# Kernel optimization log

Measured on AMD Instinct MI355X. Metric: run time of the kernel, lower is better.

The kernel has to match this reference:

```python
import jax, jax.numpy as jnp
import numpy as np

NEG_INF = -1e9


def setup_inputs() -> dict:
    key = jax.random.key(0)
    ks = jax.random.split(key, 7)
    N, Q, C = 16, 4096, 77
    D, Dc, H, S = 512, 768, 8, 64
    scale = 0.02
    return {
        "query": jax.random.normal(ks[0], (N, Q, D), jnp.float32),
        "context": jax.random.normal(ks[1], (N, C, Dc), jnp.float32),
        "Wq": jax.random.normal(ks[2], (D, H, S), jnp.float32) * scale,
        "Wk": jax.random.normal(ks[3], (Dc, H, S), jnp.float32) * scale,
        "Wv": jax.random.normal(ks[4], (Dc, H, S), jnp.float32) * scale,
        "Wo": jax.random.normal(ks[5], (H, S, D), jnp.float32) * scale,
        "bo": jnp.zeros((D,), jnp.float32),
    }


def reference(query, context, Wq, Wk, Wv, Wo, bo):
    # Projections: split hidden dim into heads.
    q = jnp.einsum('NQD,DHS->NQHS', query, Wq)      # [N,Q,H,S]
    k = jnp.einsum('NCD,DHS->NCHS', context, Wk)    # [N,C,H,S]
    v = jnp.einsum('NCD,DHS->NCHS', context, Wv)    # [N,C,H,S]
    size_per_head = q.shape[-1]
    # Attention scores [N,H,Q,C], scaled by 1/sqrt(S).
    scores = jnp.einsum('NQHS,NCHS->NHQC', q, k) * (size_per_head ** -0.5)
    weights = jax.nn.softmax(scores, axis=3)
    out = jnp.einsum('NHQC,NCHS->NQHS', weights, v)  # [N,Q,H,S]
    # Merge heads back to model dim with output bias.
    return jnp.einsum('NQHS,HSD->NQD', out, Wo) + bo
```

## Files before the change

### kernel.cpp

```cpp
#include <hip/hip_runtime.h>

typedef unsigned short u16;
typedef unsigned int u32;
typedef __bf16 bf16_t;
typedef bf16_t bf16x8 __attribute__((ext_vector_type(8)));
typedef float floatx4 __attribute__((ext_vector_type(4)));

__device__ __forceinline__ float bf2f(u16 h) {
    union { unsigned u; float f; } v;
    v.u = ((unsigned)h) << 16;
    return v.f;
}

__device__ __forceinline__ u16 f2bf(float f) {
    union { float f; unsigned u; } v;
    v.f = f;
    unsigned r = v.u + 0x7fffu + ((v.u >> 16) & 1u);
    return (u16)(r >> 16);
}

typedef __attribute__((address_space(1))) const u32 gu32;
typedef __attribute__((address_space(3))) u32 lu32;
__device__ __forceinline__ void gload16(const void* g, void* l) {
    __builtin_amdgcn_global_load_lds((gu32*)g, (lu32*)l, 16, 0, 0);
}

__global__ void transpose_all(const float* __restrict__ Wq,
                              const float* __restrict__ Wk,
                              const float* __restrict__ Wv,
                              const float* __restrict__ Wo,
                              u16* __restrict__ WqT,
                              u16* __restrict__ WkvT,
                              u16* __restrict__ WoT,
                              u16* __restrict__ vt) {
    int idx = blockIdx.x * 256 + threadIdx.x;
    if (idx < 262144) {
        int nrow = idx >> 9, k = idx & 511;
        WqT[idx] = f2bf(Wq[k * 512 + nrow] * 0.125f);
    } else if (idx < 1048576) {
        int i = idx - 262144;
        int nrow = i / 768, k = i - nrow * 768;
        WkvT[i] = f2bf((nrow < 512) ? Wk[k * 512 + nrow]
                                    : Wv[k * 512 + (nrow - 512)]);
    } else if (idx < 1310720) {
        int i = idx - 1048576;
        int nrow = i >> 9, k = i & 511;
        WoT[i] = f2bf(Wo[k * 512 + nrow]);
    } else if (idx < 2097152) {
        vt[idx - 1310720] = 0;
    }
}

#define TM 128
#define TN 256
#define TK 32

template <bool A_F32, bool OUT_F32, bool VT_SCATTER>
__device__ __forceinline__ void gemm_body(
    char* smem, const void* __restrict__ A_, const u16* __restrict__ Bt,
    void* __restrict__ C_, const float* __restrict__ bias,
    u16* __restrict__ vt,
    int M, int K, int N, int ntl2, int wg, int nwg)
{
    constexpr int AB = A_F32 ? TM * TK * 4 : TM * TK * 2;
    constexpr int BB = TN * TK * 2;

    const int tid  = threadIdx.x;
    const int lane = tid & 63;
    const int wave = tid >> 6;
    const int quad = lane >> 4;
    const int l16  = lane & 15;
    const int wm   = (wave & 1) * 64;
    const int wn   = (wave >> 1) * 64;

    const int t   = (wg & 7) * (nwg >> 3) + (wg >> 3);
    const long bm = (long)(t >> ntl2) * TM;
    const long bn = (long)(t & ((1 << ntl2) - 1)) * TN;

    const float* Af = (const float*)A_;
    const u16*   Ab = (const u16*)A_;
    const long   Mm1 = (long)M - 1;

    floatx4 acc[4][4] = {};

    auto stage = [&](int b, int k0) {
        char* Abase = smem + b * (AB + BB);
        u16*  Bb    = (u16*)(Abase + AB);
        #pragma unroll
        for (int p = 0; p < 2; ++p) {
            int ch  = p * 512 + tid;
            int row = ch >> 2;
            int pc  = (ch & 3) ^ ((row >> 1) & 3);
            gload16(Bt + (bn + row) * K + k0 + pc * 8,
                    Bb + (p * 512 + wave * 64) * 8);
        }
        if (A_F32) {
            #pragma unroll
            for (int p = 0; p < 2; ++p) {
                int ch  = p * 512 + tid;
                int row = ch >> 3;
                int pcs = (ch & 7) ^ (row & 7);
                long gr = bm + row; if (gr > Mm1) gr = Mm1;
                gload16(Af + gr * K + k0 + pcs * 4,
                        (float*)Abase + (p * 512 + wave * 64) * 4);
            }
        } else {
            int row = tid >> 2;
            int pc  = (tid & 3) ^ ((row >> 1) & 3);
            long gr = bm + row; if (gr > Mm1) gr = Mm1;
            gload16(Ab + gr * K + k0 + pc * 8,
                    (u16*)Abase + (wave * 64) * 8);
        }
    };

    const int nk = K / TK;
    stage(0, 0);

    for (int tt = 0; tt < nk; ++tt) {
        const int cb = tt & 1;
        if (tt + 1 < nk) {
            stage(cb ^ 1, (tt + 1) * TK);
            if (A_F32) asm volatile("s_waitcnt vmcnt(4)" ::: "memory");
            else       asm volatile("s_waitcnt vmcnt(3)" ::: "memory");
        } else {
            asm volatile("s_waitcnt vmcnt(0)" ::: "memory");
        }
        __builtin_amdgcn_s_barrier();
        __builtin_amdgcn_sched_barrier(0);

        const char* Abase = smem + cb * (AB + BB);
        const u16*  Bb    = (const u16*)(Abase + AB);

        bf16x8 af[4], bfr[4];
        #pragma unroll
        for (int i = 0; i < 4; ++i) {
            int row = wm + i * 16 + l16;
            if (A_F32) {
                const char* arow = Abase + (size_t)row * 128;
                int x = row & 7;
                float4 f0 = *(const float4*)(arow + (((quad * 2)     ^ x) * 16));
                float4 f1 = *(const float4*)(arow + (((quad * 2 + 1) ^ x) * 16));
                union { bf16_t h[8]; bf16x8 v; } pk;
                pk.h[0] = (bf16_t)f0.x; pk.h[1] = (bf16_t)f0.y;
                pk.h[2] = (bf16_t)f0.z; pk.h[3] = (bf16_t)f0.w;
                pk.h[4] = (bf16_t)f1.x; pk.h[5] = (bf16_t)f1.y;
                pk.h[6] = (bf16_t)f1.z; pk.h[7] = (bf16_t)f1.w;
                af[i] = pk.v;
            } else {
                int pcs = quad ^ ((row >> 1) & 3);
                af[i] = *(const bf16x8*)((const u16*)Abase + row * 32 + pcs * 8);
            }
        }
        #pragma unroll
        for (int j = 0; j < 4; ++j) {
            int row = wn + j * 16 + l16;
            int pcs = quad ^ ((row >> 1) & 3);
            bfr[j] = *(const bf16x8*)(Bb + row * 32 + pcs * 8);
        }
        #pragma unroll
        for (int i = 0; i < 4; ++i)
            #pragma unroll
            for (int j = 0; j < 4; ++j)
                acc[i][j] = __builtin_amdgcn_mfma_f32_16x16x32_bf16(
                    af[i], bfr[j], acc[i][j], 0, 0, 0);

        __builtin_amdgcn_s_barrier();
    }

    #pragma unroll
    for (int i = 0; i < 4; ++i) {
        #pragma unroll
        for (int r = 0; r < 4; ++r) {
            long row = bm + wm + i * 16 + quad * 4 + r;
            if (row >= M) continue;
            #pragma unroll
            for (int j = 0; j < 4; ++j) {
                long col = bn + wn + j * 16 + l16;
                float val = acc[i][j][r];
                if (bias) val += bias[col];
                if (VT_SCATTER && col >= 512) {
                    int n_ = (int)(row / 77);
                    int c_ = (int)(row - (long)n_ * 77);
                    int hs = (int)col - 512;
                    vt[((long)(n_ * 8 + (hs >> 6)) * 64 + (hs & 63)) * 96 + c_]
                        = f2bf(val);
                } else if (OUT_F32) {
                    ((float*)C_)[row * N + col] = val;
                } else {
                    ((u16*)C_)[row * N + col] = f2bf(val);
                }
            }
        }
    }
}

__global__ __launch_bounds__(512, 4) void proj_fused(
    const float* __restrict__ query,   const u16* __restrict__ WqT,
    u16* __restrict__ q_ws,
    const float* __restrict__ context, const u16* __restrict__ WkvT,
    u16* __restrict__ kv_ws,           u16* __restrict__ vt)
{
    __shared__ __align__(16) char smem[2 * (TM * TK * 4 + TN * TK * 2)];
    if (blockIdx.x < 80)
        gemm_body<true, false, true>(smem, context, WkvT, kv_ws, nullptr, vt,
                                     1232, 768, 1024, 2, blockIdx.x, 80);
    else
        gemm_body<true, false, false>(smem, query, WqT, q_ws, nullptr, nullptr,
                                      65536, 512, 512, 1, blockIdx.x - 80, 1024);
}

template <bool OUT_F32>
__global__ __launch_bounds__(512, 2) void gemm256(
    const u16* __restrict__ A, const u16* __restrict__ Bt,
    void* __restrict__ C_, const float* __restrict__ bias,
    int M, int K, int N, int ntl2)
{
    __shared__ u16 As[2][256 * 64];
    __shared__ u16 Bs[2][256 * 64];

    const int tid  = threadIdx.x;
    const int lane = tid & 63;
    const int wave = tid >> 6;
    const int quad = lane >> 4;
    const int l16  = lane & 15;
    const int wr   = wave & 1;
    const int wc   = wave >> 1;

    const int nwg = gridDim.x;
    const int wg  = blockIdx.x;
    const int t   = (wg & 7) * (nwg >> 3) + (wg >> 3);
    const long bm = (long)(t >> ntl2) * 256;
    const long bn = (long)(t & ((1 << ntl2) - 1)) * 256;

    floatx4 acc[8][4] = {};

    auto stage = [&](int b, int k0) {
        #pragma unroll
        for (int p = 0; p < 4; ++p) {
            int ch = p * 512 + tid;
            int r  = ch >> 3;
            int cs = (ch & 7) ^ (r & 7);
            gload16(A + (bm + r) * K + k0 + cs * 8,
                    &As[b][(p * 512 + wave * 64) * 8]);
        }
        #pragma unroll
        for (int p = 0; p < 4; ++p) {
            int ch = p * 512 + tid;
            int r  = ch >> 3;
            int cs = (ch & 7) ^ (r & 7);
            gload16(Bt + (bn + r) * K + k0 + cs * 8,
                    &Bs[b][(p * 512 + wave * 64) * 8]);
        }
    };

    const int nk = K >> 6;
    stage(0, 0);
    asm volatile("s_waitcnt vmcnt(0)" ::: "memory");
    __builtin_amdgcn_s_barrier();

    for (int tt = 0; tt < nk; ++tt) {
        const int cb = tt & 1;
        const u16* Ab = As[cb];
        const u16* Bb = Bs[cb];

        bf16x8 bfr[4][2];

        #pragma unroll
        for (int p = 0; p < 4; ++p) {
            bf16x8 af[2][2];
            #pragma unroll
            for (int ii = 0; ii < 2; ++ii) {
                int row = wr * 128 + (p * 2 + ii) * 16 + l16;
                #pragma unroll
                for (int kk = 0; kk < 2; ++kk)
                    af[ii][kk] = *(const bf16x8*)(
                        Ab + row * 64 + (((kk * 4) + quad) ^ (row & 7)) * 8);
            }
            if (p == 0) {
                #pragma unroll
                for (int j = 0; j < 4; ++j) {
                    int row = wc * 64 + j * 16 + l16;
                    #pragma unroll
                    for (int kk = 0; kk < 2; ++kk)
                        bfr[j][kk] = *(const bf16x8*)(
                            Bb + row * 64 + (((kk * 4) + quad) ^ (row & 7)) * 8);
                }
                if (tt + 1 < nk) stage(cb ^ 1, (tt + 1) << 6);
            }
            asm volatile("s_waitcnt lgkmcnt(0)" ::: "memory");
            __builtin_amdgcn_sched_barrier(0);
            __builtin_amdgcn_s_setprio(1);
            #pragma unroll
            for (int ii = 0; ii < 2; ++ii)
                #pragma unroll
                for (int j = 0; j < 4; ++j)
                    #pragma unroll
                    for (int kk = 0; kk < 2; ++kk)
                        acc[p * 2 + ii][j] = __builtin_amdgcn_mfma_f32_16x16x32_bf16(
                            af[ii][kk], bfr[j][kk], acc[p * 2 + ii][j], 0, 0, 0);
            __builtin_amdgcn_s_setprio(0);
            if (p == 3)
                asm volatile("s_waitcnt vmcnt(0)" ::: "memory");
            __builtin_amdgcn_s_barrier();
        }
    }

    float bj[4];
    #pragma unroll
    for (int j = 0; j < 4; ++j)
        bj[j] = bias ? bias[bn + wc * 64 + j * 16 + l16] : 0.f;

    #pragma unroll
    for (int i = 0; i < 8; ++i) {
        #pragma unroll
        for (int r = 0; r < 4; ++r) {
            long row = bm + wr * 128 + i * 16 + quad * 4 + r;
            #pragma unroll
            for (int j = 0; j < 4; ++j) {
                long col = bn + wc * 64 + j * 16 + l16;
                float val = acc[i][j][r] + bj[j];
                if (OUT_F32) ((float*)C_)[row * N + col] = val;
                else         ((u16*)C_)[row * N + col] = f2bf(val);
            }
        }
    }
}

__global__ __launch_bounds__(512, 4) void attn_kernel(
    const u16* __restrict__ qb,
    const u16* __restrict__ kvb,
    const u16* __restrict__ vt,
    u16* __restrict__ ob)
{
    const int QL = 4096, HS = 512;
    const int q0 = blockIdx.x * 256;
    const int h  = blockIdx.y;
    const int n  = blockIdx.z;

    __shared__ u16 ks [80 * 72];
    __shared__ u16 vts[64 * 104];
    __shared__ u16 pS [8][32 * 104];

    const int tid  = threadIdx.x;
    const int lane = tid & 63;
    const int wave = tid >> 6;
    const int quad = lane >> 4;
    const int l16  = lane & 15;

    const long qrow = (long)n * QL + q0 + wave * 32;
    bf16x8 aq[2][2];
    #pragma unroll
    for (int t = 0; t < 2; ++t)
        #pragma unroll
        for (int kk = 0; kk < 2; ++kk)
            aq[t][kk] = *(const bf16x8*)(
                qb + (qrow + t * 16 + l16) * HS + h * 64 + kk * 32 + quad * 8);

    const u16* kbase = kvb + (long)n * 77 * 1024 + h * 64;
    for (int v = tid; v < 640; v += 512) {
        int c = v >> 3, g = (v & 7) * 8;
        uint4 val = make_uint4(0, 0, 0, 0);
        if (c < 77) val = *(const uint4*)(kbase + (long)c * 1024 + g);
        *(uint4*)(&ks[c * 72 + g]) = val;
    }
    const u16* vtbase = vt + (long)((n * 8 + h) * 64) * 96;
    for (int v = tid; v < 768; v += 512) {
        int r = v / 12, c8 = v - r * 12;
        *(uint4*)(&vts[r * 104 + c8 * 8]) = *(const uint4*)(vtbase + v * 8);
    }
    __syncthreads();

    floatx4 accS[2][5] = {};
    #pragma unroll
    for (int kk = 0; kk < 2; ++kk) {
        bf16x8 bk[5];
        #pragma unroll
        for (int j = 0; j < 5; ++j)
            bk[j] = *(const bf16x8*)(&ks[(j * 16 + l16) * 72 + kk * 32 + quad * 8]);
        __builtin_amdgcn_s_setprio(1);
        #pragma unroll
        for (int t = 0; t < 2; ++t)
            #pragma unroll
            for (int j = 0; j < 5; ++j)
                accS[t][j] = __builtin_amdgcn_mfma_f32_16x16x32_bf16(
                    aq[t][kk], bk[j], accS[t][j], 0, 0, 0);
        __builtin_amdgcn_s_setprio(0);
    }

    const bool v4ok = (l16 < 13);
    u16* pw = pS[wave];
    #pragma unroll
    for (int t = 0; t < 2; ++t) {
        #pragma unroll
        for (int r = 0; r < 4; ++r) {
            float v0 = accS[t][0][r];
            float v1 = accS[t][1][r];
            float v2 = accS[t][2][r];
            float v3 = accS[t][3][r];
            float v4 = v4ok ? accS[t][4][r] : -1e30f;
            float mx = fmaxf(fmaxf(fmaxf(v0, v1), fmaxf(v2, v3)), v4);
            mx = fmaxf(mx, __shfl_xor(mx, 1));
            mx = fmaxf(mx, __shfl_xor(mx, 2));
            mx = fmaxf(mx, __shfl_xor(mx, 4));
            mx = fmaxf(mx, __shfl_xor(mx, 8));
            float e0 = __expf(v0 - mx), e1 = __expf(v1 - mx);
            float e2 = __expf(v2 - mx), e3 = __expf(v3 - mx);
            float e4 = __expf(v4 - mx);
            float sum = e0 + e1 + e2 + e3 + e4;
            sum += __shfl_xor(sum, 1);
            sum += __shfl_xor(sum, 2);
            sum += __shfl_xor(sum, 4);
            sum += __shfl_xor(sum, 8);
            float inv = 1.f / sum;
            int row = t * 16 + quad * 4 + r;
            pw[row * 104 +  0 + l16] = f2bf(e0 * inv);
            pw[row * 104 + 16 + l16] = f2bf(e1 * inv);
            pw[row * 104 + 32 + l16] = f2bf(e2 * inv);
            pw[row * 104 + 48 + l16] = f2bf(e3 * inv);
            pw[row * 104 + 64 + l16] = f2bf(e4 * inv);
            pw[row * 104 + 80 + l16] = 0;
        }
    }

    floatx4 accO[2][4] = {};
    #pragma unroll
    for (int kk = 0; kk < 3; ++kk) {
        bf16x8 aw[2], bv[4];
        #pragma unroll
        for (int t = 0; t < 2; ++t)
            aw[t] = *(const bf16x8*)(&pw[(t * 16 + l16) * 104 + kk * 32 + quad * 8]);
        #pragma unroll
        for (int j = 0; j < 4; ++j)
            bv[j] = *(const bf16x8*)(&vts[(j * 16 + l16) * 104 + kk * 32 + quad * 8]);
        __builtin_amdgcn_s_setprio(1);
        #pragma unroll
        for (int t = 0; t < 2; ++t)
            #pragma unroll
            for (int j = 0; j < 4; ++j)
                accO[t][j] = __builtin_amdgcn_mfma_f32_16x16x32_bf16(
                    aw[t], bv[j], accO[t][j], 0, 0, 0);
        __builtin_amdgcn_s_setprio(0);
    }

    #pragma unroll
    for (int t = 0; t < 2; ++t)
        #pragma unroll
        for (int j = 0; j < 4; ++j)
            #pragma unroll
            for (int r = 0; r < 4; ++r) {
                int row = t * 16 + quad * 4 + r;
                pw[row * 72 + j * 16 + l16] = f2bf(accO[t][j][r]);
            }

    u16* obase = ob + qrow * HS + h * 64;
    #pragma unroll
    for (int k = 0; k < 4; ++k) {
        int v   = k * 64 + lane;
        int row = v >> 3;
        int c8  = v & 7;
        *(uint4*)(obase + (long)row * HS + c8 * 8) =
            *(const uint4*)(&pw[row * 72 + c8 * 8]);
    }
}

extern "C" void kernel_launch(void* const* d_in, const int* in_sizes, int n_in,
                              void* d_out, int out_size, void* d_ws, size_t ws_size,
                              hipStream_t stream) {
    const float* query   = (const float*)d_in[0];
    const float* context = (const float*)d_in[1];
    const float* Wq      = (const float*)d_in[2];
    const float* Wk      = (const float*)d_in[3];
    const float* Wv      = (const float*)d_in[4];
    const float* Wo      = (const float*)d_in[5];
    const float* bo      = (const float*)d_in[6];
    float* out = (float*)d_out;

    u16* q_ws  = (u16*)d_ws;
    u16* kv_ws = q_ws + 33554432;
    u16* WqT   = kv_ws + 1261568;
    u16* WkvT  = WqT + 262144;
    u16* WoT   = WkvT + 786432;

    u16* vt = (u16*)d_out;

    transpose_all<<<dim3(8192), 256, 0, stream>>>(
        Wq, Wk, Wv, Wo, WqT, WkvT, WoT, vt);

    proj_fused<<<dim3(1104), 512, 0, stream>>>(
        query, WqT, q_ws, context, WkvT, kv_ws, vt);

    attn_kernel<<<dim3(16, 8, 16), 512, 0, stream>>>(q_ws, kv_ws, vt, q_ws);

    gemm256<true><<<dim3(512), 512, 0, stream>>>(
        q_ws, WoT, (void*)out, bo, 65536, 512, 512, 1);
}
```

Measured before the change: 375.5 us.

## Stage fp32 A tiles through registers, convert to bf16 before LDS store

```diff
diff --git a/kernel.cpp b/kernel.cpp
--- a/kernel.cpp
+++ b/kernel.cpp
@@ -55,14 +55,14 @@
 #define TN 256
 #define TK 32
 
-template <bool A_F32, bool OUT_F32, bool VT_SCATTER>
-__device__ __forceinline__ void gemm_body(
-    char* smem, const void* __restrict__ A_, const u16* __restrict__ Bt,
+template <bool OUT_F32, bool VT_SCATTER>
+__device__ __forceinline__ void gemm_body_rs(
+    char* smem, const float* __restrict__ A, const u16* __restrict__ Bt,
     void* __restrict__ C_, const float* __restrict__ bias,
     u16* __restrict__ vt,
     int M, int K, int N, int ntl2, int wg, int nwg)
 {
-    constexpr int AB = A_F32 ? TM * TK * 4 : TM * TK * 2;
+    constexpr int AB = TM * TK * 2;
     constexpr int BB = TN * TK * 2;
 
     const int tid  = threadIdx.x;
@@ -77,15 +77,32 @@
     const long bm = (long)(t >> ntl2) * TM;
     const long bn = (long)(t & ((1 << ntl2) - 1)) * TN;
 
-    const float* Af = (const float*)A_;
-    const u16*   Ab = (const u16*)A_;
-    const long   Mm1 = (long)M - 1;
+    const long Mm1 = (long)M - 1;
+
+    const int  arow = tid >> 2;
+    const int  ac   = tid & 3;
+    const int  apc  = ac ^ ((arow >> 1) & 3);
+    long agr = bm + arow; if (agr > Mm1) agr = Mm1;
+    const float* abase = A + agr * K + ac * 8;
 
     floatx4 acc[4][4] = {};
-
-    auto stage = [&](int b, int k0) {
-        char* Abase = smem + b * (AB + BB);
-        u16*  Bb    = (u16*)(Abase + AB);
+    float4 ar0, ar1;
+
+    auto issueA = [&](int k0) {
+        const float* ap = abase + k0;
+        ar0 = *(const float4*)ap;
+        ar1 = *(const float4*)(ap + 4);
+    };
+    auto writeA = [&](int b) {
+        union { bf16_t h[8]; uint4 u; } pk;
+        pk.h[0] = (bf16_t)ar0.x; pk.h[1] = (bf16_t)ar0.y;
+        pk.h[2] = (bf16_t)ar0.z; pk.h[3] = (bf16_t)ar0.w;
+        pk.h[4] = (bf16_t)ar1.x; pk.h[5] = (bf16_t)ar1.y;
+        pk.h[6] = (bf16_t)ar1.z; pk.h[7] = (bf16_t)ar1.w;
+        *(uint4*)((u16*)(smem + b * (AB + BB)) + arow * 32 + apc * 8) = pk.u;
+    };
+    auto issueB = [&](int b, int k0) {
+        u16* Bb = (u16*)(smem + b * (AB + BB) + AB);
         #pragma unroll
         for (int p = 0; p < 2; ++p) {
             int ch  = p * 512 + tid;
@@ -94,62 +111,32 @@
             gload16(Bt + (bn + row) * K + k0 + pc * 8,
                     Bb + (p * 512 + wave * 64) * 8);
         }
-        if (A_F32) {
-            #pragma unroll
-            for (int p = 0; p < 2; ++p) {
-                int ch  = p * 512 + tid;
-                int row = ch >> 3;
-                int pcs = (ch & 7) ^ (row & 7);
-                long gr = bm + row; if (gr > Mm1) gr = Mm1;
-                gload16(Af + gr * K + k0 + pcs * 4,
-                        (float*)Abase + (p * 512 + wave * 64) * 4);
-            }
-        } else {
-            int row = tid >> 2;
-            int pc  = (tid & 3) ^ ((row >> 1) & 3);
-            long gr = bm + row; if (gr > Mm1) gr = Mm1;
-            gload16(Ab + gr * K + k0 + pc * 8,
-                    (u16*)Abase + (wave * 64) * 8);
-        }
     };
 
     const int nk = K / TK;
-    stage(0, 0);
+    issueA(0);
+    issueB(0, 0);
+    writeA(0);
+    asm volatile("s_waitcnt vmcnt(0)" ::: "memory");
+    __builtin_amdgcn_s_barrier();
 
     for (int tt = 0; tt < nk; ++tt) {
         const int cb = tt & 1;
-        if (tt + 1 < nk) {
-            stage(cb ^ 1, (tt + 1) * TK);
-            if (A_F32) asm volatile("s_waitcnt vmcnt(4)" ::: "memory");
-            else       asm volatile("s_waitcnt vmcnt(3)" ::: "memory");
-        } else {
-            asm volatile("s_waitcnt vmcnt(0)" ::: "memory");
-        }
-        __builtin_amdgcn_s_barrier();
-        __builtin_amdgcn_sched_barrier(0);
-
-        const char* Abase = smem + cb * (AB + BB);
-        const u16*  Bb    = (const u16*)(Abase + AB);
+        const bool more = (tt + 1 < nk);
+        if (more) {
+            issueA((tt + 1) * TK);
+            issueB(cb ^ 1, (tt + 1) * TK);
+        }
+
+        const u16* Ab = (const u16*)(smem + cb * (AB + BB));
+        const u16* Bb = (const u16*)(smem + cb * (AB + BB) + AB);
 
         bf16x8 af[4], bfr[4];
         #pragma unroll
         for (int i = 0; i < 4; ++i) {
             int row = wm + i * 16 + l16;
-            if (A_F32) {
-                const char* arow = Abase + (size_t)row * 128;
-                int x = row & 7;
-                float4 f0 = *(const float4*)(arow + (((quad * 2)     ^ x) * 16));
-                float4 f1 = *(const float4*)(arow + (((quad * 2 + 1) ^ x) * 16));
-                union { bf16_t h[8]; bf16x8 v; } pk;
-                pk.h[0] = (bf16_t)f0.x; pk.h[1] = (bf16_t)f0.y;
-                pk.h[2] = (bf16_t)f0.z; pk.h[3] = (bf16_t)f0.w;
-                pk.h[4] = (bf16_t)f1.x; pk.h[5] = (bf16_t)f1.y;
-                pk.h[6] = (bf16_t)f1.z; pk.h[7] = (bf16_t)f1.w;
-                af[i] = pk.v;
-            } else {
-                int pcs = quad ^ ((row >> 1) & 3);
-                af[i] = *(const bf16x8*)((const u16*)Abase + row * 32 + pcs * 8);
-            }
+            int pcs = quad ^ ((row >> 1) & 3);
+            af[i] = *(const bf16x8*)(Ab + row * 32 + pcs * 8);
         }
         #pragma unroll
         for (int j = 0; j < 4; ++j) {
@@ -164,7 +151,11 @@
                 acc[i][j] = __builtin_amdgcn_mfma_f32_16x16x32_bf16(
                     af[i], bfr[j], acc[i][j], 0, 0, 0);
 
-        __builtin_amdgcn_s_barrier();
+        if (more) {
+            writeA(cb ^ 1);
+            asm volatile("s_waitcnt vmcnt(0)" ::: "memory");
+            __builtin_amdgcn_s_barrier();
+        }
     }
 
     #pragma unroll
@@ -194,19 +185,19 @@
     }
 }
 
-__global__ __launch_bounds__(512, 4) void proj_fused(
+__global__ __launch_bounds__(512, 6) void proj_fused(
     const float* __restrict__ query,   const u16* __restrict__ WqT,
     u16* __restrict__ q_ws,
     const float* __restrict__ context, const u16* __restrict__ WkvT,
     u16* __restrict__ kv_ws,           u16* __restrict__ vt)
 {
-    __shared__ __align__(16) char smem[2 * (TM * TK * 4 + TN * TK * 2)];
+    __shared__ __align__(16) char smem[2 * (TM * TK * 2 + TN * TK * 2)];
     if (blockIdx.x < 80)
-        gemm_body<true, false, true>(smem, context, WkvT, kv_ws, nullptr, vt,
-                                     1232, 768, 1024, 2, blockIdx.x, 80);
+        gemm_body_rs<false, true>(smem, context, WkvT, kv_ws, nullptr, vt,
+                                  1232, 768, 1024, 2, blockIdx.x, 80);
     else
-        gemm_body<true, false, false>(smem, query, WqT, q_ws, nullptr, nullptr,
-                                      65536, 512, 512, 1, blockIdx.x - 80, 1024);
+        gemm_body_rs<false, false>(smem, query, WqT, q_ws, nullptr, nullptr,
+                                   65536, 512, 512, 1, blockIdx.x - 80, 1024);
 }
 
 template <bool OUT_F32>
```

Result: slower. 606.0 us (+61.4%).
